# Optimization experiments

Measured on AMD Instinct MI355X. Metric: run time of the kernel, lower is better.

## Reference

```python
import jax, jax.numpy as jnp
import numpy as np

K = 3          # pred_ks
EMB_SCALE = 1.0


def _unfold(x, k):
    # torch nn.Unfold(kernel=k, padding=(k-1)//2, stride=1), channel-major (C, kh, kw)
    B, C, H, W = x.shape
    p = (k - 1) // 2
    xp = jnp.pad(x, ((0, 0), (0, 0), (p, p), (p, p)))
    pats = jnp.stack([xp[:, :, i:i + H, j:j + W] for i in range(k) for j in range(k)], axis=2)
    return pats.reshape(B, C * k * k, H, W)


def _gs2d_nearest(x, grid):
    # F.grid_sample(mode='nearest', padding_mode='zeros', align_corners=False)
    B, C, H, W = x.shape
    ix = jnp.round((grid[..., 0] + 1.0) * W / 2.0 - 0.5)
    iy = jnp.round((grid[..., 1] + 1.0) * H / 2.0 - 0.5)
    valid = (ix >= 0) & (ix <= W - 1) & (iy >= 0) & (iy <= H - 1)
    ixc = jnp.clip(ix, 0, W - 1).astype(jnp.int32)
    iyc = jnp.clip(iy, 0, H - 1).astype(jnp.int32)

    def samp(img, yy, xx, vv):
        return jnp.where(vv[None], img[:, yy, xx], 0.0)

    return jax.vmap(samp)(x, iyc, ixc, valid)


def _gs3d_trilinear(vol, coords):
    # F.grid_sample 3D, mode='bilinear', padding_mode='zeros', align_corners=False
    # vol [C,D,H,W]; coords [N,3] with (x->W, y->H, z->D)
    C, D, H, W = vol.shape
    x = (coords[:, 0] + 1.0) * W / 2.0 - 0.5
    y = (coords[:, 1] + 1.0) * H / 2.0 - 0.5
    z = (coords[:, 2] + 1.0) * D / 2.0 - 0.5
    x0, y0, z0 = jnp.floor(x), jnp.floor(y), jnp.floor(z)
    vol_f = vol.reshape(C, D * H * W)
    out = jnp.zeros((C, coords.shape[0]), vol.dtype)
    for dz in (0.0, 1.0):
        for dy in (0.0, 1.0):
            for dx in (0.0, 1.0):
                xi, yi, zi = x0 + dx, y0 + dy, z0 + dz
                wgt = (1.0 - jnp.abs(x - xi)) * (1.0 - jnp.abs(y - yi)) * (1.0 - jnp.abs(z - zi))
                valid = (xi >= 0) & (xi <= W - 1) & (yi >= 0) & (yi <= H - 1) & (zi >= 0) & (zi <= D - 1)
                idx = (jnp.clip(zi, 0, D - 1) * (H * W) + jnp.clip(yi, 0, H - 1) * W
                       + jnp.clip(xi, 0, W - 1)).astype(jnp.int32)
                out = out + vol_f[:, idx] * jnp.where(valid, wgt, 0.0)[None]
    return out


def setup_inputs() -> dict:
    key = jax.random.key(0)
    ks = jax.random.split(key, 7)
    B, H, W = 4, 64, 64
    NV, VL, NS = 16, 4, 16
    f = jnp.float32
    grid1 = jax.random.uniform(ks[0], (B, H, W, 2), f, -1.0, 1.0)
    grid2 = jax.random.uniform(ks[1], (B, H, W, 2), f, -1.0, 1.0)
    theta = jax.random.uniform(ks[2], (B,), f, -np.pi, np.pi)
    lgn = jax.random.normal(ks[3], (B, NV * VL, H, W), f)
    coefx = jax.random.uniform(ks[4], (NV, VL, VL, NS), f, -0.1, 0.1)
    coefy = jax.random.uniform(ks[5], (NV, VL, VL, NS), f, -0.1, 0.1)
    coefr = jax.random.uniform(ks[6], (NV, VL, VL, NS), f, -0.1, 0.1)
    return {"grid1": grid1, "grid2": grid2, "theta": theta, "lgn": lgn,
            "coefx": coefx, "coefy": coefy, "coefr": coefr}


def reference(grid1, grid2, theta, lgn, coefx, coefy, coefr):
    B, C, H, W = lgn.shape
    NV, VL, _, NS = coefx.shape
    KS2 = K * K
    # unfold + rearrange to [b, c*ks2, h, w]
    uf_lgn = _unfold(lgn, K)
    uf_g1 = _unfold(jnp.transpose(grid1, (0, 3, 1, 2)), K)
    # nearest-neighbor warps by grid2
    uf_lgn_t = _gs2d_nearest(uf_lgn, grid2)
    uf_g1_t = _gs2d_nearest(uf_g1, grid2)
    g1 = uf_g1_t.reshape(B, 2, KS2, H, W)
    g2 = jnp.transpose(grid2, (0, 3, 1, 2))[:, :, None]          # [b,2,1,h,w]
    d = (g2 - g1) * EMB_SCALE                                    # [b,2,ks2,h,w]
    d = jnp.transpose(d, (0, 2, 3, 4, 1)).reshape(B, KS2 * H * W, 2)
    th = jnp.broadcast_to((theta / np.pi)[:, None, None], (B, KS2 * H * W, 1))
    coords = jnp.concatenate([d, th], axis=-1).reshape(B * KS2 * H * W, 3)
    # separable coefficient volume: x along H-axis, y along D-axis, r along W-axis
    w1 = jnp.einsum('ijkn,iklm->ijlmn', coefx, coefy)            # (nv,vl,vl,D,H)
    coef = jnp.einsum('ijkmn,iklo->ijlmno', w1, coefr)           # (nv,vl,vl,D,H,W)
    vol = coef.reshape(NV * VL * VL, NS, NS, NS)
    samples = _gs3d_trilinear(vol, coords)                       # [nv*vl*vl, b*ks2*h*w]
    coef_ = samples.reshape(NV, VL, VL, B, KS2, H * W)
    coef_ = jnp.transpose(coef_, (3, 5, 4, 0, 1, 2))             # [b,hw,ks2,nv,vl,vl]
    lgn_ = uf_lgn_t.reshape(B, NV, VL, KS2, H * W)
    lgn_ = jnp.transpose(lgn_, (0, 4, 3, 1, 2))                  # [b,hw,ks2,nv,vl]
    pred = jnp.einsum('bsknij,bsknj->bsni', coef_, lgn_)         # matmul + sum over ks2
    return jnp.transpose(pred, (0, 2, 3, 1)).reshape(B, NV * VL, H, W)
```

## Files before the change

kernel.cpp:

```cpp
#include <hip/hip_runtime.h>
#include <cstdint>

#define BB   4
#define IH   64
#define IW   64
#define HWN  (IH*IW)
#define NVN  16
#define VLN  4
#define NSN  16
#define ROWP 20


__global__ __launch_bounds__(256) void transpose_lgn(const float* __restrict__ lgn,
                                                     float* __restrict__ lgnT)
{
    __shared__ float tile[64][65];
    const int b      = blockIdx.x >> 6;
    const int hwbase = (blockIdx.x & 63) << 6;
    const int t  = threadIdx.x;
    const int r0 = t >> 6;
    const int x0 = t & 63;
    const float* src = lgn + (size_t)b * (64 * HWN);
    #pragma unroll
    for (int i = 0; i < 16; ++i) {
        const int c = r0 + i * 4;
        tile[c][x0] = src[c * HWN + hwbase + x0];
    }
    __syncthreads();
    float* dst = lgnT + (size_t)b * (HWN * 64);
    #pragma unroll
    for (int i = 0; i < 16; ++i) {
        const int hw = r0 + i * 4;
        dst[(hwbase + hw) * 64 + x0] = tile[x0][hw];
    }
}

__global__ __launch_bounds__(256) void seprot_kernel(
    const float* __restrict__ grid1,
    const float* __restrict__ grid2,
    const float* __restrict__ theta,
    const float* __restrict__ lgnT,
    const float* __restrict__ coefx,
    const float* __restrict__ coefy,
    const float* __restrict__ coefr,
    float* __restrict__ out)
{
    __shared__ __align__(16) float  sE[NSN * ROWP];
    __shared__ __align__(16) float  sC[NSN * ROWP];
    __shared__ __align__(16) float2 sG1[HWN];

    const int t    = threadIdx.x;
    const int gtid = blockIdx.x * 256 + t;
    const int nv   = gtid >> 14;
    const int rem  = gtid & 16383;
    const int b    = rem >> 12;
    const int hw   = rem & 4095;

    {
        const int axis = t >> 4, sub = t & 15;
        sC[axis * ROWP + sub] = coefr[nv * 256 + sub * 16 + axis];
    }
    {
        const int n = t >> 4, e = t & 15, j = e >> 2, k2 = e & 3;
        const float th  = theta[b] / 3.14159265358979323846f;
        const float zf  = (th + 1.0f) * (0.5f * NSN) - 0.5f;
        const float zfl = floorf(zf);
        const float fz  = zf - zfl;
        const int   m0  = (int)zfl;
        const float wz0 = (m0 >= 0 && m0 <= NSN - 1) ? (1.0f - fz) : 0.0f;
        const float wz1 = (m0 + 1 >= 0 && m0 + 1 <= NSN - 1) ? fz : 0.0f;
        const int   m0c = min(max(m0, 0), NSN - 1);
        const int   m1c = min(max(m0 + 1, 0), NSN - 1);
        float eacc = 0.0f;
        #pragma unroll
        for (int k1 = 0; k1 < 4; ++k1) {
            const float a  = coefx[nv * 256 + (j * 4 + k1) * 16 + n];
            const float bm = wz0 * coefy[nv * 256 + (k1 * 4 + k2) * 16 + m0c]
                           + wz1 * coefy[nv * 256 + (k1 * 4 + k2) * 16 + m1c];
            eacc += a * bm;
        }
        sE[n * ROWP + e] = eacc;
    }
    {
        const float4* src = (const float4*)(grid1 + (size_t)b * (HWN * 2));
        float4*       dst = (float4*)sG1;
        #pragma unroll
        for (int k = 0; k < 8; ++k)
            dst[t + 256 * k] = src[t + 256 * k];
    }
    __syncthreads();

    const float2 g2  = ((const float2*)grid2)[b * HWN + hw];
    const float  sxf = rintf((g2.x + 1.0f) * (0.5f * IW) - 0.5f);
    const float  syf = rintf((g2.y + 1.0f) * (0.5f * IH) - 0.5f);
    const bool valid = (sxf >= 0.0f) && (sxf <= (float)(IW - 1)) &&
                       (syf >= 0.0f) && (syf <= (float)(IH - 1));

    const int obase = (b * (NVN * VLN) + nv * VLN) * HWN + hw;

    if (!valid) {
        #pragma unroll
        for (int j = 0; j < 4; ++j) out[obase + j * HWN] = 0.0f;
        return;
    }

    const int sx = (int)sxf, sy = (int)syf;

    float4 lgv[9];
    float2 g1t[9];
    const float4* lgb = (const float4*)lgnT + (size_t)b * (HWN * 16) + nv;
    #pragma unroll
    for (int tap = 0; tap < 9; ++tap) {
        const int di = tap / 3 - 1, dj = tap % 3 - 1;
        const int ty = sy + di, tx = sx + dj;
        const bool inb = ((unsigned)ty < (unsigned)IH) && ((unsigned)tx < (unsigned)IW);
        const int pix = min(max(ty, 0), IH - 1) * IW + min(max(tx, 0), IW - 1);
        float4 lv = lgb[pix * 16];
        const float s = inb ? 1.0f : 0.0f;
        lv.x *= s; lv.y *= s; lv.z *= s; lv.w *= s;
        lgv[tap] = lv;
        g1t[tap] = sG1[pix];
    }

    float acc[4] = {0.0f, 0.0f, 0.0f, 0.0f};
    #pragma unroll
    for (int tap = 0; tap < 9; ++tap) {
        const float dxc = g2.x - g1t[tap].x;
        const float dyc = g2.y - g1t[tap].y;

        const float xf  = (dxc + 1.0f) * (0.5f * NSN) - 0.5f;
        const float xfl = floorf(xf);
        const float fx  = xf - xfl;
        const int   o0  = (int)xfl;
        const float wx0 = (o0 >= 0 && o0 <= NSN - 1) ? (1.0f - fx) : 0.0f;
        const float wx1 = (o0 + 1 >= 0 && o0 + 1 <= NSN - 1) ? fx : 0.0f;
        const int   o0c = min(max(o0, 0), NSN - 1);
        const int   o1c = min(max(o0 + 1, 0), NSN - 1);

        const float yf  = (dyc + 1.0f) * (0.5f * NSN) - 0.5f;
        const float yfl = floorf(yf);
        const float fy  = yf - yfl;
        const int   n0  = (int)yfl;
        const float wy0 = (n0 >= 0 && n0 <= NSN - 1) ? (1.0f - fy) : 0.0f;
        const float wy1 = (n0 + 1 >= 0 && n0 + 1 <= NSN - 1) ? fy : 0.0f;
        const int   n0c = min(max(n0, 0), NSN - 1);
        const int   n1c = min(max(n0 + 1, 0), NSN - 1);

        const float lg[4] = { lgv[tap].x, lgv[tap].y, lgv[tap].z, lgv[tap].w };

        const float* cr0 = &sC[o0c * ROWP];
        const float* cr1 = &sC[o1c * ROWP];
        float v[4];
        #pragma unroll
        for (int k2 = 0; k2 < 4; ++k2) {
            float s = 0.0f;
            #pragma unroll
            for (int l = 0; l < 4; ++l)
                s += (wx0 * cr0[k2 * 4 + l] + wx1 * cr1[k2 * 4 + l]) * lg[l];
            v[k2] = s;
        }
        const float* e0 = &sE[n0c * ROWP];
        const float* e1 = &sE[n1c * ROWP];
        #pragma unroll
        for (int j = 0; j < 4; ++j) {
            float s = 0.0f;
            #pragma unroll
            for (int k2 = 0; k2 < 4; ++k2)
                s += (wy0 * e0[j * 4 + k2] + wy1 * e1[j * 4 + k2]) * v[k2];
            acc[j] += s;
        }
    }

    #pragma unroll
    for (int j = 0; j < 4; ++j)
        out[obase + j * HWN] = acc[j];
}

extern "C" void kernel_launch(void* const* d_in, const int* in_sizes, int n_in,
                              void* d_out, int out_size, void* d_ws, size_t ws_size,
                              hipStream_t stream) {
    const float* grid1 = (const float*)d_in[0];
    const float* grid2 = (const float*)d_in[1];
    const float* theta = (const float*)d_in[2];
    const float* lgn   = (const float*)d_in[3];
    const float* coefx = (const float*)d_in[4];
    const float* coefy = (const float*)d_in[5];
    const float* coefr = (const float*)d_in[6];
    float*       outp  = (float*)d_out;
    float*       lgnT  = (float*)d_ws;

    hipLaunchKernelGGL(transpose_lgn, dim3(BB * 64), dim3(256), 0, stream, lgn, lgnT);

    const int total = BB * HWN * NVN;
    hipLaunchKernelGGL(seprot_kernel, dim3(total / 256), dim3(256), 0, stream,
                       grid1, grid2, theta, lgnT, coefx, coefy, coefr, outp);
}
```

Baseline: 92.04 us.

## Switch to fp16 packed math, precompute coefficient tables, remap threads per pixel

Converts the transposed lgn buffer and the E/C coefficient tables to half precision and computes them once in a merged prep kernel, instead of recomputing E and C in every block. The main kernel now maps the 16 nv values onto adjacent lanes of one pixel, so the nine gathered taps and grid1 reads are shared across lanes and served from cache. The per-block 32KB grid1 shared-memory copy is removed. Inner contractions use packed __hfma2 arithmetic, which halves the bytes moved and the instruction count but lowers accuracy to fp16. Output stores now scatter across nv rows instead of being coalesced along hw.

```diff
diff --git a/kernel.cpp b/kernel.cpp
--- a/kernel.cpp
+++ b/kernel.cpp
@@ -1,92 +1,111 @@
 #include <hip/hip_runtime.h>
+#include <hip/hip_fp16.h>
 #include <cstdint>
 
 #define BB   4
 #define IH   64
 #define IW   64
-#define HWN  (IH*IW)
+#define HWN  4096
 #define NVN  16
-#define VLN  4
 #define NSN  16
-#define ROWP 20
-
-
-__global__ __launch_bounds__(256) void transpose_lgn(const float* __restrict__ lgn,
-                                                     float* __restrict__ lgnT)
+
+
+#define EWS_OFF  (BB*HWN*64*2)
+#define CWS_OFF  (EWS_OFF + BB*NVN*NSN*16*2)
+
+struct __align__(16) H2x4 { __half2 h[4]; };
+struct __align__(8)  H2x2 { __half2 a, b; };
+
+__global__ __launch_bounds__(256) void prep_kernel(
+    const float* __restrict__ lgn, const float* __restrict__ theta,
+    const float* __restrict__ coefx, const float* __restrict__ coefy,
+    const float* __restrict__ coefr, char* __restrict__ ws)
 {
-    __shared__ float tile[64][65];
-    const int b      = blockIdx.x >> 6;
-    const int hwbase = (blockIdx.x & 63) << 6;
-    const int t  = threadIdx.x;
-    const int r0 = t >> 6;
-    const int x0 = t & 63;
-    const float* src = lgn + (size_t)b * (64 * HWN);
-    #pragma unroll
-    for (int i = 0; i < 16; ++i) {
-        const int c = r0 + i * 4;
-        tile[c][x0] = src[c * HWN + hwbase + x0];
-    }
-    __syncthreads();
-    float* dst = lgnT + (size_t)b * (HWN * 64);
-    #pragma unroll
-    for (int i = 0; i < 16; ++i) {
-        const int hw = r0 + i * 4;
-        dst[(hwbase + hw) * 64 + x0] = tile[x0][hw];
+    const int blk = blockIdx.x, t = threadIdx.x;
+    if (blk < 256) {
+        __shared__ float tile[64][65];
+        const int b = blk >> 6, hwbase = (blk & 63) << 6;
+        const float* src = lgn + (size_t)b * (64 * HWN);
+        const int r0 = t >> 6, x0 = t & 63;
+        #pragma unroll
+        for (int i = 0; i < 16; ++i) {
+            const int c = r0 + i * 4;
+            tile[c][x0] = src[c * HWN + hwbase + x0];
+        }
+        __syncthreads();
+        __half2* dst = (__half2*)ws + (size_t)b * (HWN * 32);
+        const int cp = t & 31, hwo = t >> 5;
+        #pragma unroll
+        for (int it = 0; it < 8; ++it) {
+            const int hw = hwo + it * 8;
+            dst[(hwbase + hw) * 32 + cp] =
+                __floats2half2_rn(tile[2 * cp][hw], tile[2 * cp + 1][hw]);
+        }
+    } else if (blk < 288) {
+        const int p  = (blk - 256) * 256 + t;
+        const int b  = p >> 11, nv = (p >> 7) & 15, n = (p >> 3) & 15, q = p & 7;
+        const float th  = theta[b] * 0.31830988618379067154f;
+        const float zf  = (th + 1.0f) * 8.0f - 0.5f;
+        const float zfl = floorf(zf);
+        const float fz  = zf - zfl;
+        const int   m0  = (int)zfl;
+        const float wz0 = (m0 >= 0 && m0 <= 15) ? (1.0f - fz) : 0.0f;
+        const float wz1 = (m0 + 1 >= 0 && m0 + 1 <= 15) ? fz : 0.0f;
+        const int   m0c = min(max(m0, 0), 15), m1c = min(max(m0 + 1, 0), 15);
+        float ev[2];
+        #pragma unroll
+        for (int s = 0; s < 2; ++s) {
+            const int idx = 2 * q + s, j = idx >> 2, k2 = idx & 3;
+            float e = 0.0f;
+            #pragma unroll
+            for (int k1 = 0; k1 < 4; ++k1) {
+                const float a  = coefx[nv * 256 + (j * 4 + k1) * 16 + n];
+                const float bm = wz0 * coefy[nv * 256 + (k1 * 4 + k2) * 16 + m0c]
+                               + wz1 * coefy[nv * 256 + (k1 * 4 + k2) * 16 + m1c];
+                e += a * bm;
+            }
+            ev[s] = e;
+        }
+        ((__half2*)(ws + EWS_OFF))[p] = __floats2half2_rn(ev[0], ev[1]);
+    } else {
+        const int p = (blk - 288) * 256 + t;
+        if (p < 2048) {
+            const int nv = p >> 7, o = (p >> 3) & 15, q = p & 7;
+            const float c0 = coefr[nv * 256 + (2 * q + 0) * 16 + o];
+            const float c1 = coefr[nv * 256 + (2 * q + 1) * 16 + o];
+            ((__half2*)(ws + CWS_OFF))[p] = __floats2half2_rn(c0, c1);
+        }
     }
 }
 
 __global__ __launch_bounds__(256) void seprot_kernel(
     const float* __restrict__ grid1,
     const float* __restrict__ grid2,
-    const float* __restrict__ theta,
-    const float* __restrict__ lgnT,
-    const float* __restrict__ coefx,
-    const float* __restrict__ coefy,
-    const float* __restrict__ coefr,
+    const char*  __restrict__ ws,
     float* __restrict__ out)
 {
-    __shared__ __align__(16) float  sE[NSN * ROWP];
-    __shared__ __align__(16) float  sC[NSN * ROWP];
-    __shared__ __align__(16) float2 sG1[HWN];
-
-    const int t    = threadIdx.x;
-    const int gtid = blockIdx.x * 256 + t;
-    const int nv   = gtid >> 14;
-    const int rem  = gtid & 16383;
-    const int b    = rem >> 12;
-    const int hw   = rem & 4095;
+    __shared__ H2x4 sC[768];
+    __shared__ H2x4 sE[768];
+
+    const int t   = threadIdx.x;
+    const int blk = blockIdx.x;
+    const int b      = blk >> 8;
+    const int hwbase = (blk & 255) << 4;
+    const int pg = t >> 4;
+    const int nv = t & 15;
+    const int hw = hwbase + pg;
 
     {
-        const int axis = t >> 4, sub = t & 15;
-        sC[axis * ROWP + sub] = coefr[nv * 256 + sub * 16 + axis];
-    }
-    {
-        const int n = t >> 4, e = t & 15, j = e >> 2, k2 = e & 3;
-        const float th  = theta[b] / 3.14159265358979323846f;
-        const float zf  = (th + 1.0f) * (0.5f * NSN) - 0.5f;
-        const float zfl = floorf(zf);
-        const float fz  = zf - zfl;
-        const int   m0  = (int)zfl;
-        const float wz0 = (m0 >= 0 && m0 <= NSN - 1) ? (1.0f - fz) : 0.0f;
-        const float wz1 = (m0 + 1 >= 0 && m0 + 1 <= NSN - 1) ? fz : 0.0f;
-        const int   m0c = min(max(m0, 0), NSN - 1);
-        const int   m1c = min(max(m0 + 1, 0), NSN - 1);
-        float eacc = 0.0f;
-        #pragma unroll
-        for (int k1 = 0; k1 < 4; ++k1) {
-            const float a  = coefx[nv * 256 + (j * 4 + k1) * 16 + n];
-            const float bm = wz0 * coefy[nv * 256 + (k1 * 4 + k2) * 16 + m0c]
-                           + wz1 * coefy[nv * 256 + (k1 * 4 + k2) * 16 + m1c];
-            eacc += a * bm;
-        }
-        sE[n * ROWP + e] = eacc;
-    }
-    {
-        const float4* src = (const float4*)(grid1 + (size_t)b * (HWN * 2));
-        float4*       dst = (float4*)sG1;
-        #pragma unroll
-        for (int k = 0; k < 8; ++k)
-            dst[t + 256 * k] = src[t + 256 * k];
+        const H2x4* Cw = (const H2x4*)(ws + CWS_OFF);
+        const H2x4* Ew = (const H2x4*)(ws + EWS_OFF) + b * 512;
+        #pragma unroll
+        for (int k = 0; k < 2; ++k) {
+            const int i  = t + k * 256;
+            const int wnv = i >> 5, wo = (i >> 1) & 15, wu = i & 1;
+            const int du = wo * 48 + wnv * 3 + wu;
+            sC[du] = Cw[i];
+            sE[du] = Ew[i];
+        }
     }
     __syncthreads();
 
@@ -96,7 +115,7 @@
     const bool valid = (sxf >= 0.0f) && (sxf <= (float)(IW - 1)) &&
                        (syf >= 0.0f) && (syf <= (float)(IH - 1));
 
-    const int obase = (b * (NVN * VLN) + nv * VLN) * HWN + hw;
+    const int obase = (b * 64 + nv * 4) * HWN + hw;
 
     if (!valid) {
         #pragma unroll
@@ -105,28 +124,23 @@
     }
 
     const int sx = (int)sxf, sy = (int)syf;
-
-    float4 lgv[9];
-    float2 g1t[9];
-    const float4* lgb = (const float4*)lgnT + (size_t)b * (HWN * 16) + nv;
+    const __half2 zero2 = __floats2half2_rn(0.0f, 0.0f);
+    float acc[4] = {0.0f, 0.0f, 0.0f, 0.0f};
+
     #pragma unroll
     for (int tap = 0; tap < 9; ++tap) {
         const int di = tap / 3 - 1, dj = tap % 3 - 1;
         const int ty = sy + di, tx = sx + dj;
         const bool inb = ((unsigned)ty < (unsigned)IH) && ((unsigned)tx < (unsigned)IW);
         const int pix = min(max(ty, 0), IH - 1) * IW + min(max(tx, 0), IW - 1);
-        float4 lv = lgb[pix * 16];
-        const float s = inb ? 1.0f : 0.0f;
-        lv.x *= s; lv.y *= s; lv.z *= s; lv.w *= s;
-        lgv[tap] = lv;
-        g1t[tap] = sG1[pix];
-    }
-
-    float acc[4] = {0.0f, 0.0f, 0.0f, 0.0f};
-    #pragma unroll
-    for (int tap = 0; tap < 9; ++tap) {
-        const float dxc = g2.x - g1t[tap].x;
-        const float dyc = g2.y - g1t[tap].y;
+
+        H2x2 lgu = ((const H2x2*)ws)[(b * HWN + pix) * 16 + nv];
+        __half2 lg01 = inb ? lgu.a : zero2;
+        __half2 lg23 = inb ? lgu.b : zero2;
+
+        const float2 g1 = ((const float2*)grid1)[b * HWN + pix];
+        const float dxc = g2.x - g1.x;
+        const float dyc = g2.y - g1.y;
 
         const float xf  = (dxc + 1.0f) * (0.5f * NSN) - 0.5f;
         const float xfl = floorf(xf);
@@ -146,28 +160,46 @@
         const int   n0c = min(max(n0, 0), NSN - 1);
         const int   n1c = min(max(n0 + 1, 0), NSN - 1);
 
-        const float lg[4] = { lgv[tap].x, lgv[tap].y, lgv[tap].z, lgv[tap].w };
-
-        const float* cr0 = &sC[o0c * ROWP];
-        const float* cr1 = &sC[o1c * ROWP];
-        float v[4];
+        const __half2 wx0h = __floats2half2_rn(wx0, wx0);
+        const __half2 wx1h = __floats2half2_rn(wx1, wx1);
+        const __half2 wy0h = __floats2half2_rn(wy0, wy0);
+        const __half2 wy1h = __floats2half2_rn(wy1, wy1);
+
+        const H2x4 c0a = sC[o0c * 48 + nv * 3 + 0];
+        const H2x4 c0b = sC[o0c * 48 + nv * 3 + 1];
+        const H2x4 c1a = sC[o1c * 48 + nv * 3 + 0];
+        const H2x4 c1b = sC[o1c * 48 + nv * 3 + 1];
+        __half2 bl[8];
+        #pragma unroll
+        for (int k = 0; k < 4; ++k) {
+            bl[k]     = __hfma2(c0a.h[k], wx0h, __hmul2(c1a.h[k], wx1h));
+            bl[4 + k] = __hfma2(c0b.h[k], wx0h, __hmul2(c1b.h[k], wx1h));
+        }
+        float vf[4];
         #pragma unroll
         for (int k2 = 0; k2 < 4; ++k2) {
-            float s = 0.0f;
-            #pragma unroll
-            for (int l = 0; l < 4; ++l)
-                s += (wx0 * cr0[k2 * 4 + l] + wx1 * cr1[k2 * 4 + l]) * lg[l];
-            v[k2] = s;
-        }
-        const float* e0 = &sE[n0c * ROWP];
-        const float* e1 = &sE[n1c * ROWP];
+            const __half2 sv = __hfma2(bl[2 * k2 + 1], lg23,
+                                       __hmul2(bl[2 * k2], lg01));
+            vf[k2] = __low2float(sv) + __high2float(sv);
+        }
+        const __half2 v01 = __floats2half2_rn(vf[0], vf[1]);
+        const __half2 v23 = __floats2half2_rn(vf[2], vf[3]);
+
+        const H2x4 e0a = sE[n0c * 48 + nv * 3 + 0];
+        const H2x4 e0b = sE[n0c * 48 + nv * 3 + 1];
+        const H2x4 e1a = sE[n1c * 48 + nv * 3 + 0];
+        const H2x4 e1b = sE[n1c * 48 + nv * 3 + 1];
+        __half2 eb[8];
+        #pragma unroll
+        for (int k = 0; k < 4; ++k) {
+            eb[k]     = __hfma2(e0a.h[k], wy0h, __hmul2(e1a.h[k], wy1h));
+            eb[4 + k] = __hfma2(e0b.h[k], wy0h, __hmul2(e1b.h[k], wy1h));
+        }
         #pragma unroll
         for (int j = 0; j < 4; ++j) {
-            float s = 0.0f;
-            #pragma unroll
-            for (int k2 = 0; k2 < 4; ++k2)
-                s += (wy0 * e0[j * 4 + k2] + wy1 * e1[j * 4 + k2]) * v[k2];
-            acc[j] += s;
+            const __half2 sa = __hfma2(eb[2 * j + 1], v23,
+                                       __hmul2(eb[2 * j], v01));
+            acc[j] += __low2float(sa) + __high2float(sa);
         }
     }
 
@@ -187,11 +219,11 @@
     const float* coefy = (const float*)d_in[5];
     const float* coefr = (const float*)d_in[6];
     float*       outp  = (float*)d_out;
-    float*       lgnT  = (float*)d_ws;
-
-    hipLaunchKernelGGL(transpose_lgn, dim3(BB * 64), dim3(256), 0, stream, lgn, lgnT);
-
-    const int total = BB * HWN * NVN;
-    hipLaunchKernelGGL(seprot_kernel, dim3(total / 256), dim3(256), 0, stream,
-                       grid1, grid2, theta, lgnT, coefx, coefy, coefr, outp);
+    char*        ws    = (char*)d_ws;
+
+    hipLaunchKernelGGL(prep_kernel, dim3(296), dim3(256), 0, stream,
+                       lgn, theta, coefx, coefy, coefr, ws);
+
+    hipLaunchKernelGGL(seprot_kernel, dim3(BB * 256), dim3(256), 0, stream,
+                       grid1, grid2, ws, outp);
 }
```

New measurement: 82.68 us. 1.11x faster.
